# Kernel optimization log

Hardware: AMD Instinct MI355X
Metric: run time of the kernel (lower is better)

Reference implementation:

```python
import jax, jax.numpy as jnp
import numpy as np


def setup_inputs() -> dict:
    key = jax.random.key(0)
    ks = jax.random.split(key, 4)
    B, L, E = 2, 2048, 512
    scale = 0.02
    return {
        "x": jax.random.normal(ks[0], (B, L, E), dtype=jnp.float32),
        "Wq": jax.random.normal(ks[1], (E, E), dtype=jnp.float32) * scale,
        "bq": jnp.zeros((E,), dtype=jnp.float32),
        "Wk": jax.random.normal(ks[2], (E, E), dtype=jnp.float32) * scale,
        "bk": jnp.zeros((E,), dtype=jnp.float32),
        "Wv": jax.random.normal(ks[3], (E, E), dtype=jnp.float32) * scale,
        "bv": jnp.zeros((E,), dtype=jnp.float32),
        "window_size": 64,
    }


def reference(x, Wq, bq, Wk, bk, Wv, bv, window_size):
    # x: [B, L, E]; Linear weights stored torch-style as [out, in].
    B, L, E = x.shape
    q = jnp.einsum("ble,fe->blf", x, Wq) + bq  # [B, L, E]
    k = jnp.einsum("ble,fe->blf", x, Wk) + bk
    v = jnp.einsum("ble,fe->blf", x, Wv) + bv

    w = window_size
    W = 2 * w + 1
    # Window indices per query position i: [i-w, i+w], clipped; invalid masked.
    offsets = jnp.arange(-w, w + 1)                 # [W]
    idx = jnp.arange(L)[:, None] + offsets[None, :]  # [L, W]
    valid = (idx >= 0) & (idx < L)                   # [L, W]
    idx_c = jnp.clip(idx, 0, L - 1)

    k_win = k[:, idx_c]  # [B, L, W, E]
    v_win = v[:, idx_c]  # [B, L, W, E]

    scores = jnp.einsum("ble,blwe->blw", q, k_win) / jnp.sqrt(jnp.float32(E))
    scores = jnp.where(valid[None, :, :], scores, -jnp.inf)
    probs = jax.nn.softmax(scores, axis=-1)          # [B, L, W]
    out = jnp.einsum("blw,blwe->ble", probs, v_win)  # [B, L, E]
    return out
```

## Files before the change

kernel.cpp:

```cpp
#include <hip/hip_runtime.h>
#include <cstdint>
#include <cstddef>

#define L_SEQ 2048
#define E_DIM 512
#define B_SZ 2
#define WIN 64
#define SCALE_QK 0.044194173824159216f

typedef __attribute__((ext_vector_type(8))) short short8;
typedef __attribute__((ext_vector_type(4))) float floatx4;

__device__ __forceinline__ unsigned short f2bf(float f) {
    unsigned int u = __float_as_uint(f);
    u += 0x7FFFu + ((u >> 16) & 1u);
    return (unsigned short)(u >> 16);
}

__device__ __forceinline__ uint4 pk8(const float4 lo, const float4 hi) {
    uint4 r;
    asm("v_cvt_pk_bf16_f32 %0, %1, %2" : "=v"(r.x) : "v"(lo.x), "v"(lo.y));
    asm("v_cvt_pk_bf16_f32 %0, %1, %2" : "=v"(r.y) : "v"(lo.z), "v"(lo.w));
    asm("v_cvt_pk_bf16_f32 %0, %1, %2" : "=v"(r.z) : "v"(hi.x), "v"(hi.y));
    asm("v_cvt_pk_bf16_f32 %0, %1, %2" : "=v"(r.w) : "v"(hi.z), "v"(hi.w));
    return r;
}

__device__ __forceinline__ void ld16cvt(const float* g, uint4& r0, uint4& r1) {
    float4 f0 = *(const float4*)(g);
    float4 f1 = *(const float4*)(g + 4);
    float4 f2 = *(const float4*)(g + 8);
    float4 f3 = *(const float4*)(g + 12);
    r0 = pk8(f0, f1);
    r1 = pk8(f2, f3);
}

#define ALD 72
__global__ __launch_bounds__(256) void qkv_gemm(
    const float* __restrict__ x,
    const float* __restrict__ Wq, const float* __restrict__ Wk, const float* __restrict__ Wv,
    const float* __restrict__ bq, const float* __restrict__ bk, const float* __restrict__ bv,
    unsigned short* __restrict__ q, unsigned short* __restrict__ k,
    unsigned short* __restrict__ vt)
{
    __shared__ __align__(16) unsigned short As[64 * ALD];
    __shared__ __align__(16) unsigned short Bs[64 * ALD];

    const int t = threadIdx.x;
    const int w = t >> 6, l = t & 63;
    const int m0 = blockIdx.x * 64, n0 = blockIdx.y * 64, z = blockIdx.z;
    const float* W    = (z == 0) ? Wq : ((z == 1) ? Wk : Wv);
    const float* bias = (z == 0) ? bq : ((z == 1) ? bk : bv);

    floatx4 acc[2][2] = {};
    const int wm = (w >> 1) * 32, wn = (w & 1) * 32;
    const int fr = l & 15, fq = l >> 4, fk = fq * 8;

    const int srow = t >> 2, scol = (t & 3) * 16;
    const float* gA = x + (size_t)(m0 + srow) * 512 + scol;
    const float* gB = W + (size_t)(n0 + srow) * 512 + scol;

    uint4 ra0, ra1, rb0, rb1;
    ld16cvt(gA, ra0, ra1);
    ld16cvt(gB, rb0, rb1);

    for (int it = 0; it < 8; it++) {
        *(uint4*)&As[srow * ALD + scol]     = ra0;
        *(uint4*)&As[srow * ALD + scol + 8] = ra1;
        *(uint4*)&Bs[srow * ALD + scol]     = rb0;
        *(uint4*)&Bs[srow * ALD + scol + 8] = rb1;
        __syncthreads();
        if (it < 7) {
            int kk = (it + 1) * 64;
            ld16cvt(gA + kk, ra0, ra1);
            ld16cvt(gB + kk, rb0, rb1);
        }
        short8 a[2][2], bf[2][2];
#pragma unroll
        for (int i = 0; i < 2; i++)
#pragma unroll
            for (int kh = 0; kh < 2; kh++)
                a[i][kh] = *(const short8*)&As[(wm + i * 16 + fr) * ALD + kh * 32 + fk];
#pragma unroll
        for (int j = 0; j < 2; j++)
#pragma unroll
            for (int kh = 0; kh < 2; kh++)
                bf[j][kh] = *(const short8*)&Bs[(wn + j * 16 + fr) * ALD + kh * 32 + fk];
#pragma unroll
        for (int kh = 0; kh < 2; kh++)
#pragma unroll
            for (int i = 0; i < 2; i++)
#pragma unroll
                for (int j = 0; j < 2; j++)
                    acc[i][j] = __builtin_amdgcn_mfma_f32_16x16x32_bf16(a[i][kh], bf[j][kh], acc[i][j], 0, 0, 0);
        __syncthreads();
    }

    unsigned short* Tl = As;
    float bv_[2];
#pragma unroll
    for (int j = 0; j < 2; j++) bv_[j] = bias[n0 + wn + j * 16 + fr];

    if (z < 2) {
#pragma unroll
        for (int i = 0; i < 2; i++)
#pragma unroll
            for (int j = 0; j < 2; j++)
#pragma unroll
                for (int r = 0; r < 4; r++)
                    Tl[(wm + i * 16 + fq * 4 + r) * ALD + wn + j * 16 + fr] =
                        f2bf(acc[i][j][r] + bv_[j]);
    } else {
#pragma unroll
        for (int i = 0; i < 2; i++)
#pragma unroll
            for (int j = 0; j < 2; j++)
#pragma unroll
                for (int r = 0; r < 4; r++)
                    Tl[(wn + j * 16 + fr) * ALD + wm + i * 16 + fq * 4 + r] =
                        f2bf(acc[i][j][r] + bv_[j]);
    }
    __syncthreads();

    const int tr = t >> 2, tc = (t & 3) * 16;
    uint4 v0 = *(const uint4*)&Tl[tr * ALD + tc];
    uint4 v1 = *(const uint4*)&Tl[tr * ALD + tc + 8];
    if (z < 2) {
        unsigned short* out = (z == 0) ? q : k;
        *(uint4*)&out[(size_t)(m0 + tr) * 512 + n0 + tc]     = v0;
        *(uint4*)&out[(size_t)(m0 + tr) * 512 + n0 + tc + 8] = v1;
    } else {
        *(uint4*)&vt[(size_t)(n0 + tr) * 4096 + m0 + tc]     = v0;
        *(uint4*)&vt[(size_t)(n0 + tr) * 4096 + m0 + tc + 8] = v1;
    }
}

#define SLD 164
__global__ __launch_bounds__(512) void attn_fused(
    const unsigned short* __restrict__ qb, const unsigned short* __restrict__ kb,
    const unsigned short* __restrict__ vt, float* __restrict__ out)
{
    __shared__ __align__(16) float Sl[16 * SLD];

    const int t = threadIdx.x;
    const int w = t >> 6, l = t & 63;
    const int fr = l & 15, fq = l >> 4;
    const int Q0 = blockIdx.x * 16;
    const int b  = blockIdx.y;
    const int R0 = Q0 - WIN;

    {
        const unsigned short* qrow = qb + (size_t)(b * L_SEQ + Q0 + fr) * 512 + fq * 8;
        short8 qf[16];
#pragma unroll
        for (int ks = 0; ks < 16; ks++) qf[ks] = *(const short8*)(qrow + ks * 32);

        for (int nt = w; nt < 9; nt += 8) {
            const int tok = R0 + nt * 16 + fr;
            const bool kvalid = (tok >= 0) && (tok < L_SEQ);
            const int tokc = min(max(tok, 0), L_SEQ - 1);
            const unsigned short* krow = kb + (size_t)(b * L_SEQ + tokc) * 512 + fq * 8;

            floatx4 acc0 = {}, acc1 = {};
            short8 bfr[8];
#pragma unroll
            for (int ks = 0; ks < 8; ks++) bfr[ks] = *(const short8*)(krow + ks * 32);
#pragma unroll
            for (int ks = 0; ks < 8; ks++)
                acc0 = __builtin_amdgcn_mfma_f32_16x16x32_bf16(qf[ks], bfr[ks], acc0, 0, 0, 0);
#pragma unroll
            for (int ks = 0; ks < 8; ks++) bfr[ks] = *(const short8*)(krow + (8 + ks) * 32);
#pragma unroll
            for (int ks = 0; ks < 8; ks++)
                acc1 = __builtin_amdgcn_mfma_f32_16x16x32_bf16(qf[8 + ks], bfr[ks], acc1, 0, 0, 0);

            const int jg = nt * 16 + fr;
#pragma unroll
            for (int r = 0; r < 4; r++) {
                int qq = fq * 4 + r;
                bool valid = kvalid && (jg >= qq) && (jg <= qq + 128);
                Sl[qq * SLD + jg] = valid ? (acc0[r] + acc1[r]) * SCALE_QK : -1e30f;
            }
        }
    }
    __syncthreads();

    const float* Srow = &Sl[fr * SLD + fq * 8];
    float sv[5][8];
#pragma unroll
    for (int ks = 0; ks < 5; ks++) {
        float4 u0 = *(const float4*)(Srow + ks * 32);
        float4 u1 = *(const float4*)(Srow + ks * 32 + 4);
        sv[ks][0] = u0.x; sv[ks][1] = u0.y; sv[ks][2] = u0.z; sv[ks][3] = u0.w;
        sv[ks][4] = u1.x; sv[ks][5] = u1.y; sv[ks][6] = u1.z; sv[ks][7] = u1.w;
    }
    if (fq >= 2) {
#pragma unroll
        for (int j = 0; j < 8; j++) sv[4][j] = -1e30f;
    }
    float m = -1e30f;
#pragma unroll
    for (int ks = 0; ks < 5; ks++)
#pragma unroll
        for (int j = 0; j < 8; j++) m = fmaxf(m, sv[ks][j]);
    m = fmaxf(m, __shfl_xor(m, 16));
    m = fmaxf(m, __shfl_xor(m, 32));
    float sum = 0.f;
#pragma unroll
    for (int ks = 0; ks < 5; ks++)
#pragma unroll
        for (int j = 0; j < 8; j++) { float e = __expf(sv[ks][j] - m); sv[ks][j] = e; sum += e; }
    sum += __shfl_xor(sum, 16);
    sum += __shfl_xor(sum, 32);
    float inv = 1.f / sum;

    short8 a[5];
#pragma unroll
    for (int ks = 0; ks < 5; ks++)
#pragma unroll
        for (int j = 0; j < 8; j++) a[ks][j] = (short)f2bf(sv[ks][j] * inv);

    const int EC = w * 64;
    int tkc[5];
#pragma unroll
    for (int ks = 0; ks < 5; ks++) {
        int tok0 = R0 + ks * 32 + fq * 8;
        tkc[ks] = min(max(tok0, 0), L_SEQ - 8);
    }
    floatx4 oa[4] = {};
#pragma unroll
    for (int et = 0; et < 4; et++) {
        const unsigned short* vrow = vt + (size_t)(EC + et * 16 + fr) * 4096 + b * L_SEQ;
        short8 vfr[5];
#pragma unroll
        for (int ks = 0; ks < 5; ks++) vfr[ks] = *(const short8*)(vrow + tkc[ks]);
#pragma unroll
        for (int ks = 0; ks < 5; ks++)
            oa[et] = __builtin_amdgcn_mfma_f32_16x16x32_bf16(a[ks], vfr[ks], oa[et], 0, 0, 0);
    }

    float* op = out + (size_t)b * L_SEQ * E_DIM;
#pragma unroll
    for (int et = 0; et < 4; et++)
#pragma unroll
        for (int r = 0; r < 4; r++)
            op[(size_t)(Q0 + fq * 4 + r) * 512 + EC + et * 16 + fr] = oa[et][r];
}

extern "C" void kernel_launch(void* const* d_in, const int* in_sizes, int n_in,
                              void* d_out, int out_size, void* d_ws, size_t ws_size,
                              hipStream_t stream)
{
    const float* x  = (const float*)d_in[0];
    const float* Wq = (const float*)d_in[1];
    const float* bq = (const float*)d_in[2];
    const float* Wk = (const float*)d_in[3];
    const float* bk = (const float*)d_in[4];
    const float* Wv = (const float*)d_in[5];
    const float* bv = (const float*)d_in[6];
    float* out = (float*)d_out;

    char* ws = (char*)d_ws;
    unsigned short* qb = (unsigned short*)(ws);
    unsigned short* kb = (unsigned short*)(ws + 4194304);
    unsigned short* vt = (unsigned short*)(ws + 8388608);

    qkv_gemm<<<dim3(64, 8, 3), 256, 0, stream>>>(x, Wq, Wk, Wv, bq, bk, bv, qb, kb, vt);
    attn_fused<<<dim3(128, 2), 512, 0, stream>>>(qb, kb, vt, out);
}
```

Measured before the change: 115.2 us.

## Fuse Q/K/V projections into one GEMM block reusing the x tile

The QKV projection kernel now computes all three projections in one block, loading and converting each x tile once and reusing it across Wq, Wk and Wv. This cuts redundant x loads and fp32-to-bf16 conversions, at the cost of 3x accumulator registers and fewer blocks (512 instead of 1536). The register prefetch double-buffering is dropped in favour of a simple load-store-sync loop, and launch bounds ask for 2 blocks per CU. The attention kernel also remaps block indices so that blocks launched close together work on query tiles spread across the sequence.

```diff
diff --git a/kernel.cpp b/kernel.cpp
--- a/kernel.cpp
+++ b/kernel.cpp
@@ -36,7 +36,7 @@
 }
 
 #define ALD 72
-__global__ __launch_bounds__(256) void qkv_gemm(
+__global__ __launch_bounds__(256, 2) void qkv_fused(
     const float* __restrict__ x,
     const float* __restrict__ Wq, const float* __restrict__ Wk, const float* __restrict__ Wv,
     const float* __restrict__ bq, const float* __restrict__ bk, const float* __restrict__ bv,
@@ -44,94 +44,104 @@
     unsigned short* __restrict__ vt)
 {
     __shared__ __align__(16) unsigned short As[64 * ALD];
-    __shared__ __align__(16) unsigned short Bs[64 * ALD];
+    __shared__ __align__(16) unsigned short Bs[3][64 * ALD];
 
     const int t = threadIdx.x;
     const int w = t >> 6, l = t & 63;
-    const int m0 = blockIdx.x * 64, n0 = blockIdx.y * 64, z = blockIdx.z;
-    const float* W    = (z == 0) ? Wq : ((z == 1) ? Wk : Wv);
-    const float* bias = (z == 0) ? bq : ((z == 1) ? bk : bv);
-
-    floatx4 acc[2][2] = {};
+    const int m0 = blockIdx.x * 64, n0 = blockIdx.y * 64;
+    const float* Ws[3] = { Wq, Wk, Wv };
+
+    floatx4 acc[3][2][2] = {};
     const int wm = (w >> 1) * 32, wn = (w & 1) * 32;
     const int fr = l & 15, fq = l >> 4, fk = fq * 8;
 
     const int srow = t >> 2, scol = (t & 3) * 16;
     const float* gA = x + (size_t)(m0 + srow) * 512 + scol;
-    const float* gB = W + (size_t)(n0 + srow) * 512 + scol;
-
-    uint4 ra0, ra1, rb0, rb1;
-    ld16cvt(gA, ra0, ra1);
-    ld16cvt(gB, rb0, rb1);
-
-    for (int it = 0; it < 8; it++) {
-        *(uint4*)&As[srow * ALD + scol]     = ra0;
-        *(uint4*)&As[srow * ALD + scol + 8] = ra1;
-        *(uint4*)&Bs[srow * ALD + scol]     = rb0;
-        *(uint4*)&Bs[srow * ALD + scol + 8] = rb1;
+
+    float bv_[3][2];
+    {
+        const float* bs[3] = { bq, bk, bv };
+#pragma unroll
+        for (int z = 0; z < 3; z++)
+#pragma unroll
+            for (int j = 0; j < 2; j++) bv_[z][j] = bs[z][n0 + wn + j * 16 + fr];
+    }
+
+    for (int kt = 0; kt < 8; kt++) {
+        const int kk = kt * 64;
+        uint4 r0, r1;
+        ld16cvt(gA + kk, r0, r1);
+        *(uint4*)&As[srow * ALD + scol]     = r0;
+        *(uint4*)&As[srow * ALD + scol + 8] = r1;
+#pragma unroll
+        for (int z = 0; z < 3; z++) {
+            ld16cvt(Ws[z] + (size_t)(n0 + srow) * 512 + scol + kk, r0, r1);
+            *(uint4*)&Bs[z][srow * ALD + scol]     = r0;
+            *(uint4*)&Bs[z][srow * ALD + scol + 8] = r1;
+        }
         __syncthreads();
-        if (it < 7) {
-            int kk = (it + 1) * 64;
-            ld16cvt(gA + kk, ra0, ra1);
-            ld16cvt(gB + kk, rb0, rb1);
-        }
-        short8 a[2][2], bf[2][2];
+
+        short8 a[2][2];
 #pragma unroll
         for (int i = 0; i < 2; i++)
 #pragma unroll
             for (int kh = 0; kh < 2; kh++)
                 a[i][kh] = *(const short8*)&As[(wm + i * 16 + fr) * ALD + kh * 32 + fk];
 #pragma unroll
-        for (int j = 0; j < 2; j++)
+        for (int z = 0; z < 3; z++) {
+            short8 bf[2][2];
+#pragma unroll
+            for (int j = 0; j < 2; j++)
+#pragma unroll
+                for (int kh = 0; kh < 2; kh++)
+                    bf[j][kh] = *(const short8*)&Bs[z][(wn + j * 16 + fr) * ALD + kh * 32 + fk];
 #pragma unroll
             for (int kh = 0; kh < 2; kh++)
-                bf[j][kh] = *(const short8*)&Bs[(wn + j * 16 + fr) * ALD + kh * 32 + fk];
-#pragma unroll
-        for (int kh = 0; kh < 2; kh++)
+#pragma unroll
+                for (int i = 0; i < 2; i++)
+#pragma unroll
+                    for (int j = 0; j < 2; j++)
+                        acc[z][i][j] = __builtin_amdgcn_mfma_f32_16x16x32_bf16(a[i][kh], bf[j][kh], acc[z][i][j], 0, 0, 0);
+        }
+        __syncthreads();
+    }
+
+    unsigned short* Tl = As;
+    const int tr = t >> 2, tc = (t & 3) * 16;
+#pragma unroll
+    for (int z = 0; z < 3; z++) {
+        if (z) __syncthreads();
+        if (z < 2) {
 #pragma unroll
             for (int i = 0; i < 2; i++)
 #pragma unroll
                 for (int j = 0; j < 2; j++)
-                    acc[i][j] = __builtin_amdgcn_mfma_f32_16x16x32_bf16(a[i][kh], bf[j][kh], acc[i][j], 0, 0, 0);
+#pragma unroll
+                    for (int r = 0; r < 4; r++)
+                        Tl[(wm + i * 16 + fq * 4 + r) * ALD + wn + j * 16 + fr] =
+                            f2bf(acc[z][i][j][r] + bv_[z][j]);
+        } else {
+#pragma unroll
+            for (int i = 0; i < 2; i++)
+#pragma unroll
+                for (int j = 0; j < 2; j++)
+#pragma unroll
+                    for (int r = 0; r < 4; r++)
+                        Tl[(wn + j * 16 + fr) * ALD + wm + i * 16 + fq * 4 + r] =
+                            f2bf(acc[z][i][j][r] + bv_[z][j]);
+        }
         __syncthreads();
-    }
-
-    unsigned short* Tl = As;
-    float bv_[2];
-#pragma unroll
-    for (int j = 0; j < 2; j++) bv_[j] = bias[n0 + wn + j * 16 + fr];
-
-    if (z < 2) {
-#pragma unroll
-        for (int i = 0; i < 2; i++)
-#pragma unroll
-            for (int j = 0; j < 2; j++)
-#pragma unroll
-                for (int r = 0; r < 4; r++)
-                    Tl[(wm + i * 16 + fq * 4 + r) * ALD + wn + j * 16 + fr] =
-                        f2bf(acc[i][j][r] + bv_[j]);
-    } else {
-#pragma unroll
-        for (int i = 0; i < 2; i++)
-#pragma unroll
-            for (int j = 0; j < 2; j++)
-#pragma unroll
-                for (int r = 0; r < 4; r++)
-                    Tl[(wn + j * 16 + fr) * ALD + wm + i * 16 + fq * 4 + r] =
-                        f2bf(acc[i][j][r] + bv_[j]);
-    }
-    __syncthreads();
-
-    const int tr = t >> 2, tc = (t & 3) * 16;
-    uint4 v0 = *(const uint4*)&Tl[tr * ALD + tc];
-    uint4 v1 = *(const uint4*)&Tl[tr * ALD + tc + 8];
-    if (z < 2) {
-        unsigned short* out = (z == 0) ? q : k;
-        *(uint4*)&out[(size_t)(m0 + tr) * 512 + n0 + tc]     = v0;
-        *(uint4*)&out[(size_t)(m0 + tr) * 512 + n0 + tc + 8] = v1;
-    } else {
-        *(uint4*)&vt[(size_t)(n0 + tr) * 4096 + m0 + tc]     = v0;
-        *(uint4*)&vt[(size_t)(n0 + tr) * 4096 + m0 + tc + 8] = v1;
+
+        uint4 v0 = *(const uint4*)&Tl[tr * ALD + tc];
+        uint4 v1 = *(const uint4*)&Tl[tr * ALD + tc + 8];
+        if (z < 2) {
+            unsigned short* out = (z == 0) ? q : k;
+            *(uint4*)&out[(size_t)(m0 + tr) * 512 + n0 + tc]     = v0;
+            *(uint4*)&out[(size_t)(m0 + tr) * 512 + n0 + tc + 8] = v1;
+        } else {
+            *(uint4*)&vt[(size_t)(n0 + tr) * 4096 + m0 + tc]     = v0;
+            *(uint4*)&vt[(size_t)(n0 + tr) * 4096 + m0 + tc + 8] = v1;
+        }
     }
 }
 
@@ -145,7 +155,9 @@
     const int t = threadIdx.x;
     const int w = t >> 6, l = t & 63;
     const int fr = l & 15, fq = l >> 4;
-    const int Q0 = blockIdx.x * 16;
+    const int bx = blockIdx.x;
+    const int Qt = (bx & 7) * 16 + (bx >> 3);
+    const int Q0 = Qt * 16;
     const int b  = blockIdx.y;
     const int R0 = Q0 - WIN;
 
@@ -265,6 +277,6 @@
     unsigned short* kb = (unsigned short*)(ws + 4194304);
     unsigned short* vt = (unsigned short*)(ws + 8388608);
 
-    qkv_gemm<<<dim3(64, 8, 3), 256, 0, stream>>>(x, Wq, Wk, Wv, bq, bk, bv, qb, kb, vt);
+    qkv_fused<<<dim3(64, 8), 256, 0, stream>>>(x, Wq, Wk, Wv, bq, bk, bv, qb, kb, vt);
     attn_fused<<<dim3(128, 2), 512, 0, stream>>>(qb, kb, vt, out);
 }
```

Result: faster. 112.0 us (-2.8%).
